# Performance work log

Measured on AMD Instinct MI355X. Metric: run time of the kernel, lower is better.

The kernel has to match this reference:

```python
import jax, jax.numpy as jnp
import numpy as np

LN2 = float(np.log(2.0))


def setup_inputs() -> dict:
    key = jax.random.key(0)
    k1, k2, k3 = jax.random.split(key, 3)
    B, S, F = 32, 8192, 4
    H = 256
    x = jax.random.uniform(k1, (B, S, F), dtype=jnp.float32)  # positive OHLC-like prices
    lin_w = jax.random.normal(k2, (H, 3), dtype=jnp.float32) * (1.0 / np.sqrt(3.0))
    lin_b = jax.random.normal(k3, (H,), dtype=jnp.float32) * 0.01
    return {"x": x, "lin_w": lin_w, "lin_b": lin_b, "window_size": 64}


def _volatility_measures(x, window_size):
    # x: [B, S, 4]; close at channel 3, high at 1, low at 2
    B, S, _ = x.shape
    W = window_size
    close = x[:, :, 3]                                        # [B, S]
    r = jnp.log(close[:, 1:] / close[:, :-1] + 1e-8)          # [B, S-1] log returns

    # For output time t in [W, S): window close[t-W:t] -> returns r[t-W : t-1], length W-1
    t = jnp.arange(W, S)                                      # [T], T = S - W
    idx = t[:, None] - W + jnp.arange(W - 1)[None, :]         # [T, W-1] indices into r
    rw = r[:, idx]                                            # [B, T, W-1]

    std_dev = jnp.std(rw, axis=-1, ddof=1)                    # [B, T] unbiased (torch.std)

    high = x[:, W:, 1]
    low = x[:, W:, 2]
    log_hl = jnp.log(high / low + 1e-8)                       # [B, T]

    c = 2.0 * LN2 - 1.0
    # mean over window of (0.5*log_hl^2 - c*r^2); log_hl is constant per window
    gk = jnp.sqrt(0.5 * log_hl ** 2 - c * jnp.mean(rw ** 2, axis=-1))  # [B, T]
    pk = jnp.sqrt(log_hl ** 2 / (4.0 * LN2))                  # [B, T]

    body = jnp.stack([std_dev, gk, pk], axis=-1)              # [B, T, 3]
    measures = jnp.zeros((B, S, 3), dtype=x.dtype).at[:, W:, :].set(body)
    return jnp.nan_to_num(measures)


def reference(x, lin_w, lin_b, window_size):
    measures = _volatility_measures(x, window_size)           # [B, S, 3]
    out = jnp.einsum('bsf,hf->bsh', measures, lin_w) + lin_b  # Linear(3 -> H)
    return jax.nn.relu(out)
```

## Files before the change

### kernel.cpp

```cpp
#include <hip/hip_runtime.h>

#define S 8192
#define H 256
#define W 64
#define RPB 64

typedef float v4f __attribute__((ext_vector_type(4)));

__device__ __forceinline__ float nan2num(float v) {
    const float FMAX = 3.4028234663852886e38f;
    if (v != v) return 0.0f;
    if (v > FMAX) return FMAX;
    if (v < -FMAX) return -FMAX;
    return v;
}

__global__ __launch_bounds__(256, 8) void vol_one(
    const float4* __restrict__ x,
    const float*  __restrict__ lin_w,
    const float*  __restrict__ lin_b,
    v4f*          __restrict__ out)
{
    __shared__ float s_close[RPB + W];
    __shared__ float s_r[RPB + W - 1];
    __shared__ float s_m0[RPB];
    __shared__ float s_m1[RPB];
    __shared__ float s_m2[RPB];

    const int tid = threadIdx.x;
    const size_t row0 = (size_t)blockIdx.x * RPB;
    const int b  = (int)(row0 / S);
    const int s0 = (int)(row0 % S);

    const float4* xb = x + (size_t)b * S;

    if (tid < RPB + W) {
        int j = s0 - W + tid;
        s_close[tid] = xb[j < 0 ? 0 : j].w;
    }
    __syncthreads();

    if (tid < RPB + W - 1) {
        s_r[tid] = logf(s_close[tid + 1] / s_close[tid] + 1e-8f);
    }
    __syncthreads();

    if (tid < RPB) {
        const float inv_n = 1.0f / 63.0f;
        float sum = 0.0f, sq = 0.0f;
        #pragma unroll 7
        for (int k = 0; k < W - 1; ++k) {
            float v = s_r[tid + k];
            sum += v;
            sq  = fmaf(v, v, sq);
        }
        const float mean = sum * inv_n;

        float m0 = 0.0f, m1 = 0.0f, m2 = 0.0f;
        const int t = s0 + tid;
        if (t >= W) {
            float4 hv  = xb[t];
            float lhl  = logf(hv.y / hv.z + 1e-8f);
            float var = (sq - sum * mean) * (1.0f / 62.0f);
            m0 = (var >= 0.0f) ? sqrtf(var) : 0.0f;
            float arg = 0.5f * lhl * lhl - 0.3862943611198906f * (sq * inv_n);
            m1 = (arg >= 0.0f) ? sqrtf(arg) : 0.0f;
            m2 = sqrtf(lhl * lhl * 0.3606737602222409f);
            m0 = nan2num(m0); m1 = nan2num(m1); m2 = nan2num(m2);
        }
        s_m0[tid] = m0; s_m1[tid] = m1; s_m2[tid] = m2;
    }
    __syncthreads();

    const int hq = tid & 63;
    const int wv = tid >> 6;
    const int h0 = hq * 4;

    const float wa0 = lin_w[(h0+0)*3+0], wb0 = lin_w[(h0+0)*3+1], wc0 = lin_w[(h0+0)*3+2];
    const float wa1 = lin_w[(h0+1)*3+0], wb1 = lin_w[(h0+1)*3+1], wc1 = lin_w[(h0+1)*3+2];
    const float wa2 = lin_w[(h0+2)*3+0], wb2 = lin_w[(h0+2)*3+1], wc2 = lin_w[(h0+2)*3+2];
    const float wa3 = lin_w[(h0+3)*3+0], wb3 = lin_w[(h0+3)*3+1], wc3 = lin_w[(h0+3)*3+2];
    const v4f bv = ((const v4f*)lin_b)[hq];

    v4f* op = out + (row0 + wv) * (H / 4) + hq;

    #pragma unroll 4
    for (int i = 0; i < RPB / 4; ++i) {
        const int tl = (i << 2) + wv;
        const float m0 = s_m0[tl], m1 = s_m1[tl], m2 = s_m2[tl];
        v4f o;
        o.x = fmaxf(0.0f, fmaf(m0, wa0, fmaf(m1, wb0, fmaf(m2, wc0, bv.x))));
        o.y = fmaxf(0.0f, fmaf(m0, wa1, fmaf(m1, wb1, fmaf(m2, wc1, bv.y))));
        o.z = fmaxf(0.0f, fmaf(m0, wa2, fmaf(m1, wb2, fmaf(m2, wc2, bv.z))));
        o.w = fmaxf(0.0f, fmaf(m0, wa3, fmaf(m1, wb3, fmaf(m2, wc3, bv.w))));
        op[(size_t)i * 4 * (H / 4)] = o;
    }
}

extern "C" void kernel_launch(void* const* d_in, const int* in_sizes, int n_in,
                              void* d_out, int out_size, void* d_ws, size_t ws_size,
                              hipStream_t stream) {
    const float4* x  = (const float4*)d_in[0];
    const float*  lw = (const float*)d_in[1];
    const float*  lb = (const float*)d_in[2];

    const int B = in_sizes[0] / (S * 4);
    const size_t rows = (size_t)B * S;

    hipLaunchKernelGGL(vol_one, dim3((unsigned)(rows / RPB)), dim3(256), 0, stream,
                       x, lw, lb, (v4f*)d_out);
}
```

Baseline: 46.77 us.

## Split window reduction across four lanes and drop a barrier stage

Log returns are now computed straight from global close values, which removes the s_close staging array and one __syncthreads. The 63-element window sum is split across 4 threads per row (16 elements each, with the last masked) and combined with xor shuffles, so all 256 threads take part instead of 64. The three measure arrays are packed into one v4f shared array, so the output loop reads one vector instead of three scalars. In exchange, each close value is loaded twice from global memory, and the lanes do some redundant masked work.

```diff
diff --git a/kernel.cpp b/kernel.cpp
--- a/kernel.cpp
+++ b/kernel.cpp
@@ -21,11 +21,8 @@
     const float*  __restrict__ lin_b,
     v4f*          __restrict__ out)
 {
-    __shared__ float s_close[RPB + W];
     __shared__ float s_r[RPB + W - 1];
-    __shared__ float s_m0[RPB];
-    __shared__ float s_m1[RPB];
-    __shared__ float s_m2[RPB];
+    __shared__ v4f   s_m[RPB];
 
     const int tid = threadIdx.x;
     const size_t row0 = (size_t)blockIdx.x * RPB;
@@ -34,41 +31,51 @@
 
     const float4* xb = x + (size_t)b * S;
 
-    if (tid < RPB + W) {
+    if (tid < RPB + W - 1) {
         int j = s0 - W + tid;
-        s_close[tid] = xb[j < 0 ? 0 : j].w;
+        if (j < 0) j = 0;
+        float c0 = xb[j].w;
+        float c1 = xb[j + 1].w;
+        s_r[tid] = logf(c1 / c0 + 1e-8f);
     }
     __syncthreads();
 
-    if (tid < RPB + W - 1) {
-        s_r[tid] = logf(s_close[tid + 1] / s_close[tid] + 1e-8f);
-    }
-    __syncthreads();
-
-    if (tid < RPB) {
-        const float inv_n = 1.0f / 63.0f;
+    {
+        const int r = tid >> 2;
+        const int p = tid & 3;
+        const int k0 = p * 16;
         float sum = 0.0f, sq = 0.0f;
-        #pragma unroll 7
-        for (int k = 0; k < W - 1; ++k) {
-            float v = s_r[tid + k];
+        #pragma unroll
+        for (int i = 0; i < 16; ++i) {
+            const int k = k0 + i;
+            float v = s_r[r + k];
+            v = (k == 63) ? 0.0f : v;
             sum += v;
             sq  = fmaf(v, v, sq);
         }
-        const float mean = sum * inv_n;
+        sum += __shfl_xor(sum, 1);
+        sum += __shfl_xor(sum, 2);
+        sq  += __shfl_xor(sq, 1);
+        sq  += __shfl_xor(sq, 2);
 
-        float m0 = 0.0f, m1 = 0.0f, m2 = 0.0f;
-        const int t = s0 + tid;
-        if (t >= W) {
-            float4 hv  = xb[t];
-            float lhl  = logf(hv.y / hv.z + 1e-8f);
-            float var = (sq - sum * mean) * (1.0f / 62.0f);
-            m0 = (var >= 0.0f) ? sqrtf(var) : 0.0f;
-            float arg = 0.5f * lhl * lhl - 0.3862943611198906f * (sq * inv_n);
-            m1 = (arg >= 0.0f) ? sqrtf(arg) : 0.0f;
-            m2 = sqrtf(lhl * lhl * 0.3606737602222409f);
-            m0 = nan2num(m0); m1 = nan2num(m1); m2 = nan2num(m2);
+        if (p == 0) {
+            const float inv_n = 1.0f / 63.0f;
+            float m0 = 0.0f, m1 = 0.0f, m2 = 0.0f;
+            const int t = s0 + r;
+            if (t >= W) {
+                float4 hv  = xb[t];
+                float lhl  = logf(hv.y / hv.z + 1e-8f);
+                float mean = sum * inv_n;
+                float var  = (sq - sum * mean) * (1.0f / 62.0f);
+                m0 = (var >= 0.0f) ? sqrtf(var) : 0.0f;
+                float arg = 0.5f * lhl * lhl - 0.3862943611198906f * (sq * inv_n);
+                m1 = (arg >= 0.0f) ? sqrtf(arg) : 0.0f;
+                m2 = sqrtf(lhl * lhl * 0.3606737602222409f);
+                m0 = nan2num(m0); m1 = nan2num(m1); m2 = nan2num(m2);
+            }
+            v4f mv; mv.x = m0; mv.y = m1; mv.z = m2; mv.w = 0.0f;
+            s_m[r] = mv;
         }
-        s_m0[tid] = m0; s_m1[tid] = m1; s_m2[tid] = m2;
     }
     __syncthreads();
 
@@ -86,13 +93,12 @@
 
     #pragma unroll 4
     for (int i = 0; i < RPB / 4; ++i) {
-        const int tl = (i << 2) + wv;
-        const float m0 = s_m0[tl], m1 = s_m1[tl], m2 = s_m2[tl];
+        const v4f mv = s_m[(i << 2) + wv];
         v4f o;
-        o.x = fmaxf(0.0f, fmaf(m0, wa0, fmaf(m1, wb0, fmaf(m2, wc0, bv.x))));
-        o.y = fmaxf(0.0f, fmaf(m0, wa1, fmaf(m1, wb1, fmaf(m2, wc1, bv.y))));
-        o.z = fmaxf(0.0f, fmaf(m0, wa2, fmaf(m1, wb2, fmaf(m2, wc2, bv.z))));
-        o.w = fmaxf(0.0f, fmaf(m0, wa3, fmaf(m1, wb3, fmaf(m2, wc3, bv.w))));
+        o.x = fmaxf(0.0f, fmaf(mv.x, wa0, fmaf(mv.y, wb0, fmaf(mv.z, wc0, bv.x))));
+        o.y = fmaxf(0.0f, fmaf(mv.x, wa1, fmaf(mv.y, wb1, fmaf(mv.z, wc1, bv.y))));
+        o.z = fmaxf(0.0f, fmaf(mv.x, wa2, fmaf(mv.y, wb2, fmaf(mv.z, wc2, bv.z))));
+        o.w = fmaxf(0.0f, fmaf(mv.x, wa3, fmaf(mv.y, wb3, fmaf(mv.z, wc3, bv.w))));
         op[(size_t)i * 4 * (H / 4)] = o;
     }
 }
```

Result: no change. 46.69 us (-0.2%).
